# Kernel tuning notes

Measured on AMD Instinct MI355X. Metric: run time of the kernel, lower is better.

The kernel has to match this reference:

```python
import jax, jax.numpy as jnp
import numpy as np

L, N, C = 128, 32, 128
DIM_MLP, OUT = 128, 128


def setup_inputs() -> dict:
    key = jax.random.key(0)
    ks = jax.random.split(key, 6)
    s_in2 = 1.0 / np.sqrt(2 * C)
    s_mid = 1.0 / np.sqrt(DIM_MLP)
    s_in = 1.0 / np.sqrt(C)
    return {
        "x": jax.random.normal(ks[0], (L, N, C), jnp.float32),
        "attn_w1": jax.random.normal(ks[1], (2 * C, DIM_MLP), jnp.float32) * s_in2,
        "attn_b1": jnp.zeros((DIM_MLP,), jnp.float32),
        "attn_w2": jax.random.normal(ks[2], (DIM_MLP, OUT), jnp.float32) * s_mid,
        "attn_b2": jnp.zeros((OUT,), jnp.float32),
        "value_w1": jax.random.normal(ks[3], (C, DIM_MLP), jnp.float32) * s_in,
        "value_b1": jnp.zeros((DIM_MLP,), jnp.float32),
        "value_w2": jax.random.normal(ks[4], (DIM_MLP, OUT), jnp.float32) * s_mid,
        "value_b2": jnp.zeros((OUT,), jnp.float32),
    }


def reference(x, attn_w1, attn_b1, attn_w2, attn_b2,
              value_w1, value_b1, value_w2, value_b2):
    l, n, c = x.shape
    # Outer concat: pair[i, j, b] = concat(x[i, b], x[j, b])  -> (l, l, N, 2C)
    xi = jnp.broadcast_to(x[:, None, :, :], (l, l, n, c))
    xj = jnp.broadcast_to(x[None, :, :, :], (l, l, n, c))
    pair = jnp.concatenate([xi, xj], axis=-1)
    # Pairwise attention MLP (ReLU hidden, linear output)
    h = jax.nn.relu(pair @ attn_w1 + attn_b1)          # (l, l, N, dim_mlp)
    attn = h @ attn_w2 + attn_b2                       # (l, l, N, out)
    # Value MLP
    hv = jax.nn.relu(x @ value_w1 + value_b1)          # (l, N, dim_mlp)
    value = hv @ value_w2 + value_b2                   # (l, N, out)
    # Elementwise weighted reduce over key axis j (NOT a matmul over channels)
    out = jnp.einsum('ijbc,jbc->ibc', attn, value)     # (l, N, out)
    return out
```

## Files before the change

kernel.cpp:

```cpp
#include <hip/hip_runtime.h>
#include <hip/hip_bf16.h>

#define L_DIM 128
#define N_DIM 32
#define C_DIM 128
#define K_DIM 128
#define OUT_DIM 128

#define QV_STRIDE 132

typedef __attribute__((ext_vector_type(8))) short short8;
typedef __attribute__((ext_vector_type(4))) float float4v;

static __device__ __forceinline__ short bf16_bits(float f) {
    __bf16 h = (__bf16)f;
    return __builtin_bit_cast(short, h);
}

__global__ __launch_bounds__(256) void k_pre(
    const float* __restrict__ x,
    const float* __restrict__ attn_w1, const float* __restrict__ attn_b1,
    const float* __restrict__ attn_w2,
    const float* __restrict__ value_w1, const float* __restrict__ value_b1,
    const float* __restrict__ value_w2, const float* __restrict__ value_b2,
    float* __restrict__ P, float* __restrict__ Q, float* __restrict__ V,
    short* __restrict__ W2s)
{
    int bid = blockIdx.x;
    if (bid >= 512) {
        int e = (bid - 512) * 256 + threadIdx.x;
        int idx  = e & 7;
        int colr = (e >> 3) & 15;
        int quad = (e >> 7) & 3;
        int mi   = (e >> 9) & 3;
        int ct   = e >> 11;
        int k = quad * 8 + 32 * mi + idx;
        int c = ct * 16 + colr;
        W2s[e] = bf16_bits(attn_w2[k * OUT_DIM + c]);
        return;
    }

    __shared__ float xs[8][C_DIM];
    __shared__ float hvs[8][K_DIM];
    int tid = threadIdx.x;
    int r0  = bid * 8;

    {
        int f = tid * 4;
        int row = f >> 7, c = f & 127;
        *(float4v*)(&xs[row][c]) = *(const float4v*)(x + (r0 + row) * C_DIM + c);
    }
    __syncthreads();

    int ks   = tid & 127;
    int half = tid >> 7;

    float pacc[4] = {0,0,0,0};
    float qacc[4] = {0,0,0,0};
    float hacc[4] = {0,0,0,0};
    #pragma unroll 4
    for (int c = 0; c < C_DIM; ++c) {
        float wa = attn_w1[c * K_DIM + ks];
        float wb = attn_w1[(C_DIM + c) * K_DIM + ks];
        float wv = value_w1[c * K_DIM + ks];
        #pragma unroll
        for (int r = 0; r < 4; ++r) {
            float xr = xs[half * 4 + r][c];
            pacc[r] = fmaf(xr, wa, pacc[r]);
            qacc[r] = fmaf(xr, wb, qacc[r]);
            hacc[r] = fmaf(xr, wv, hacc[r]);
        }
    }
    float b1 = attn_b1[ks], vb1 = value_b1[ks];
    #pragma unroll
    for (int r = 0; r < 4; ++r) {
        int rr = r0 + half * 4 + r;
        int i = rr >> 5, bb = rr & 31;
        P[(bb * L_DIM + i) * K_DIM + ks] = pacc[r];
        Q[(bb * L_DIM + i) * K_DIM + ks] = qacc[r] + b1;
        hvs[half * 4 + r][ks] = fmaxf(hacc[r] + vb1, 0.f);
    }
    __syncthreads();

    float vacc[4] = {0,0,0,0};
    #pragma unroll 4
    for (int k = 0; k < K_DIM; ++k) {
        float w = value_w2[k * OUT_DIM + ks];
        #pragma unroll
        for (int r = 0; r < 4; ++r)
            vacc[r] = fmaf(hvs[half * 4 + r][k], w, vacc[r]);
    }
    float vb2 = value_b2[ks];
    #pragma unroll
    for (int r = 0; r < 4; ++r) {
        int rr = r0 + half * 4 + r;
        int i = rr >> 5, bb = rr & 31;
        V[(bb * L_DIM + i) * OUT_DIM + ks] = vacc[r] + vb2;
    }
}

__global__ __launch_bounds__(256)
__attribute__((amdgpu_waves_per_eu(3)))
void k_main(
    const float* __restrict__ P, const float* __restrict__ Q,
    const float* __restrict__ V,
    const short* __restrict__ W2s, const float* __restrict__ attn_b2,
    float* __restrict__ out)
{
    __shared__ float Q_lds[2][16 * QV_STRIDE];
    __shared__ float V_lds[2][16 * QV_STRIDE];
    __shared__ float P_lds[2 * K_DIM];

    int b     = blockIdx.x >> 6;
    int ipair = blockIdx.x & 63;
    int tid   = threadIdx.x;
    int wave  = tid >> 6;
    int lane  = tid & 63;
    int quad  = lane >> 4;
    int col   = lane & 15;
    int iw    = wave >> 1;
    int cth   = wave & 1;

    short8 bfrag[4][4];
    const short8* w2p = (const short8*)W2s;
    #pragma unroll
    for (int cl = 0; cl < 4; ++cl)
        #pragma unroll
        for (int mi = 0; mi < 4; ++mi)
            bfrag[cl][mi] =
                w2p[(((cth * 4 + cl) * 4 + mi) * 4 + quad) * 16 + col];

    if (tid < 64)
        *(float4v*)&P_lds[tid * 4] =
            *(const float4v*)(P + (b * L_DIM + ipair * 2 + (tid >> 5)) * K_DIM
                              + (tid & 31) * 4);

    int srow = tid >> 4;
    int sc8  = (tid & 15) * 8;
    const float* Qbase = Q + (size_t)(b * L_DIM) * K_DIM;
    const float* Vbase = V + (size_t)(b * L_DIM) * OUT_DIM;

    {
        const float* qp = Qbase + srow * K_DIM + sc8;
        const float* vp = Vbase + srow * OUT_DIM + sc8;
        float4v qa = *(const float4v*)qp, qb = *(const float4v*)(qp + 4);
        float4v va = *(const float4v*)vp, vb = *(const float4v*)(vp + 4);
        *(float4v*)&Q_lds[0][srow * QV_STRIDE + sc8]     = qa;
        *(float4v*)&Q_lds[0][srow * QV_STRIDE + sc8 + 4] = qb;
        *(float4v*)&V_lds[0][srow * QV_STRIDE + sc8]     = va;
        *(float4v*)&V_lds[0][srow * QV_STRIDE + sc8 + 4] = vb;
    }
    __syncthreads();

    float acc[4] = {0.f, 0.f, 0.f, 0.f};
    float sv[4]  = {0.f, 0.f, 0.f, 0.f};
    const float* Pw = &P_lds[iw * K_DIM];

    for (int r = 0; r < 8; ++r) {
        int cur = r & 1;

        float4v nqa, nqb, nva, nvb;
        if (r < 7) {
            const float* qp = Qbase + ((r + 1) * 16 + srow) * K_DIM + sc8;
            const float* vp = Vbase + ((r + 1) * 16 + srow) * OUT_DIM + sc8;
            nqa = *(const float4v*)qp; nqb = *(const float4v*)(qp + 4);
            nva = *(const float4v*)vp; nvb = *(const float4v*)(vp + 4);
        }

        short8 af[4];
        const float* Qc = &Q_lds[cur][col * QV_STRIDE + quad * 8];
        #pragma unroll
        for (int ksl = 0; ksl < 4; ++ksl) {
            float4v q0 = *(const float4v*)(Qc + ksl * 32);
            float4v q1 = *(const float4v*)(Qc + ksl * 32 + 4);
            float4v p0 = *(const float4v*)(Pw + ksl * 32 + quad * 8);
            float4v p1 = *(const float4v*)(Pw + ksl * 32 + quad * 8 + 4);
            float4v s0 = p0 + q0;
            float4v s1 = p1 + q1;
            short8 a;
            #pragma unroll
            for (int t = 0; t < 4; ++t) {
                a[t]     = bf16_bits(fmaxf(s0[t], 0.f));
                a[t + 4] = bf16_bits(fmaxf(s1[t], 0.f));
            }
            af[ksl] = a;
        }

        const float* Vc = &V_lds[cur][0];
        #pragma unroll
        for (int cl = 0; cl < 4; ++cl) {
            float4v c4 = {0.f, 0.f, 0.f, 0.f};
            #pragma unroll
            for (int ksl = 0; ksl < 4; ++ksl)
                c4 = __builtin_amdgcn_mfma_f32_16x16x32_bf16(
                        af[ksl], bfrag[cl][ksl], c4, 0, 0, 0);
            int cc = cth * 64 + cl * 16 + col;
            #pragma unroll
            for (int rr = 0; rr < 4; ++rr) {
                float v = Vc[(quad * 4 + rr) * QV_STRIDE + cc];
                acc[cl] = fmaf(c4[rr], v, acc[cl]);
                sv[cl] += v;
            }
        }

        if (r < 7) {
            int nxt = cur ^ 1;
            *(float4v*)&Q_lds[nxt][srow * QV_STRIDE + sc8]     = nqa;
            *(float4v*)&Q_lds[nxt][srow * QV_STRIDE + sc8 + 4] = nqb;
            *(float4v*)&V_lds[nxt][srow * QV_STRIDE + sc8]     = nva;
            *(float4v*)&V_lds[nxt][srow * QV_STRIDE + sc8 + 4] = nvb;
            __syncthreads();
        }
    }

    #pragma unroll
    for (int cl = 0; cl < 4; ++cl) {
        acc[cl] += __shfl_xor(acc[cl], 16, 64);
        acc[cl] += __shfl_xor(acc[cl], 32, 64);
        sv[cl]  += __shfl_xor(sv[cl], 16, 64);
        sv[cl]  += __shfl_xor(sv[cl], 32, 64);
    }

    if (quad == 0) {
        int ig = ipair * 2 + iw;
        #pragma unroll
        for (int cl = 0; cl < 4; ++cl) {
            int cc = cth * 64 + cl * 16 + col;
            out[(ig * N_DIM + b) * OUT_DIM + cc] = acc[cl] + attn_b2[cc] * sv[cl];
        }
    }
}

extern "C" void kernel_launch(void* const* d_in, const int* in_sizes, int n_in,
                              void* d_out, int out_size, void* d_ws, size_t ws_size,
                              hipStream_t stream)
{
    const float* x        = (const float*)d_in[0];
    const float* attn_w1  = (const float*)d_in[1];
    const float* attn_b1  = (const float*)d_in[2];
    const float* attn_w2  = (const float*)d_in[3];
    const float* attn_b2  = (const float*)d_in[4];
    const float* value_w1 = (const float*)d_in[5];
    const float* value_b1 = (const float*)d_in[6];
    const float* value_w2 = (const float*)d_in[7];
    const float* value_b2 = (const float*)d_in[8];
    float* out = (float*)d_out;

    float* ws  = (float*)d_ws;
    float* P   = ws;
    float* Q   = ws + 524288;
    float* V   = ws + 1048576;
    short* W2s = (short*)(ws + 1572864);

    k_pre<<<576, 256, 0, stream>>>(x, attn_w1, attn_b1, attn_w2,
                                   value_w1, value_b1, value_w2, value_b2,
                                   P, Q, V, W2s);
    k_main<<<2048, 256, 0, stream>>>(P, Q, V, W2s, attn_b2, out);
}
```

Baseline: 127.4 us.

## Process two query rows per wave, transpose V layout, hold P in registers

Each wave now handles two output rows i, so every staged Q/V tile and every W2 fragment load is reused across two MFMA chains, and the grid halves to 1024 blocks. V is written transposed by the pre-kernel so each lane reads its four V values with one vector LDS load instead of four scalar loads. P moves from LDS into registers, and the pre-kernel's x indexing is regrouped per batch. This costs more registers (launch bounds changed to 2 blocks per CU) and fewer blocks to hide latency.

```diff
diff --git a/kernel.cpp b/kernel.cpp
--- a/kernel.cpp
+++ b/kernel.cpp
@@ -7,7 +7,8 @@
 #define K_DIM 128
 #define OUT_DIM 128
 
-#define QV_STRIDE 132
+#define Q_STRIDE  132
+#define VT_STRIDE 20
 
 typedef __attribute__((ext_vector_type(8))) short short8;
 typedef __attribute__((ext_vector_type(4))) float float4v;
@@ -23,7 +24,7 @@
     const float* __restrict__ attn_w2,
     const float* __restrict__ value_w1, const float* __restrict__ value_b1,
     const float* __restrict__ value_w2, const float* __restrict__ value_b2,
-    float* __restrict__ P, float* __restrict__ Q, float* __restrict__ V,
+    float* __restrict__ P, float* __restrict__ Q, float* __restrict__ Vt,
     short* __restrict__ W2s)
 {
     int bid = blockIdx.x;
@@ -43,12 +44,14 @@
     __shared__ float xs[8][C_DIM];
     __shared__ float hvs[8][K_DIM];
     int tid = threadIdx.x;
-    int r0  = bid * 8;
+    int b   = bid >> 4;
+    int i0g = (bid & 15) * 8;
 
     {
         int f = tid * 4;
         int row = f >> 7, c = f & 127;
-        *(float4v*)(&xs[row][c]) = *(const float4v*)(x + (r0 + row) * C_DIM + c);
+        *(float4v*)(&xs[row][c]) =
+            *(const float4v*)(x + ((size_t)(i0g + row) * N_DIM + b) * C_DIM + c);
     }
     __syncthreads();
 
@@ -74,10 +77,9 @@
     float b1 = attn_b1[ks], vb1 = value_b1[ks];
     #pragma unroll
     for (int r = 0; r < 4; ++r) {
-        int rr = r0 + half * 4 + r;
-        int i = rr >> 5, bb = rr & 31;
-        P[(bb * L_DIM + i) * K_DIM + ks] = pacc[r];
-        Q[(bb * L_DIM + i) * K_DIM + ks] = qacc[r] + b1;
+        int i = i0g + half * 4 + r;
+        P[((size_t)b * L_DIM + i) * K_DIM + ks] = pacc[r];
+        Q[((size_t)b * L_DIM + i) * K_DIM + ks] = qacc[r] + b1;
         hvs[half * 4 + r][ks] = fmaxf(hacc[r] + vb1, 0.f);
     }
     __syncthreads();
@@ -91,35 +93,30 @@
             vacc[r] = fmaf(hvs[half * 4 + r][k], w, vacc[r]);
     }
     float vb2 = value_b2[ks];
-    #pragma unroll
-    for (int r = 0; r < 4; ++r) {
-        int rr = r0 + half * 4 + r;
-        int i = rr >> 5, bb = rr & 31;
-        V[(bb * L_DIM + i) * OUT_DIM + ks] = vacc[r] + vb2;
-    }
-}
-
-__global__ __launch_bounds__(256)
-__attribute__((amdgpu_waves_per_eu(3)))
+    float4v vout = { vacc[0] + vb2, vacc[1] + vb2, vacc[2] + vb2, vacc[3] + vb2 };
+    *(float4v*)(Vt + ((size_t)b * OUT_DIM + ks) * L_DIM + i0g + half * 4) = vout;
+}
+
+__global__ __launch_bounds__(256, 2)
 void k_main(
     const float* __restrict__ P, const float* __restrict__ Q,
-    const float* __restrict__ V,
+    const float* __restrict__ Vt,
     const short* __restrict__ W2s, const float* __restrict__ attn_b2,
     float* __restrict__ out)
 {
-    __shared__ float Q_lds[2][16 * QV_STRIDE];
-    __shared__ float V_lds[2][16 * QV_STRIDE];
-    __shared__ float P_lds[2 * K_DIM];
-
-    int b     = blockIdx.x >> 6;
-    int ipair = blockIdx.x & 63;
-    int tid   = threadIdx.x;
-    int wave  = tid >> 6;
-    int lane  = tid & 63;
-    int quad  = lane >> 4;
-    int col   = lane & 15;
-    int iw    = wave >> 1;
-    int cth   = wave & 1;
+    __shared__ float Q_lds[2][16 * Q_STRIDE];
+    __shared__ float Vt_lds[2][128 * VT_STRIDE];
+
+    int b    = blockIdx.x >> 5;
+    int it4  = blockIdx.x & 31;
+    int tid  = threadIdx.x;
+    int wave = tid >> 6;
+    int lane = tid & 63;
+    int quad = lane >> 4;
+    int col  = lane & 15;
+    int ip   = wave >> 1;
+    int cth  = wave & 1;
+    int i0   = it4 * 4 + ip * 2;
 
     short8 bfrag[4][4];
     const short8* w2p = (const short8*)W2s;
@@ -130,31 +127,39 @@
             bfrag[cl][mi] =
                 w2p[(((cth * 4 + cl) * 4 + mi) * 4 + quad) * 16 + col];
 
-    if (tid < 64)
-        *(float4v*)&P_lds[tid * 4] =
-            *(const float4v*)(P + (b * L_DIM + ipair * 2 + (tid >> 5)) * K_DIM
-                              + (tid & 31) * 4);
+    float4v pf[2][4][2];
+    #pragma unroll
+    for (int ii = 0; ii < 2; ++ii) {
+        const float* Pp = P + ((size_t)b * L_DIM + i0 + ii) * K_DIM + quad * 8;
+        #pragma unroll
+        for (int ksl = 0; ksl < 4; ++ksl) {
+            pf[ii][ksl][0] = *(const float4v*)(Pp + ksl * 32);
+            pf[ii][ksl][1] = *(const float4v*)(Pp + ksl * 32 + 4);
+        }
+    }
 
     int srow = tid >> 4;
     int sc8  = (tid & 15) * 8;
-    const float* Qbase = Q + (size_t)(b * L_DIM) * K_DIM;
-    const float* Vbase = V + (size_t)(b * L_DIM) * OUT_DIM;
+    int cs   = tid >> 1;
+    int ch   = (tid & 1) * 8;
+    const float* Qbase = Q  + (size_t)b * L_DIM * K_DIM;
+    const float* Vbase = Vt + (size_t)b * OUT_DIM * L_DIM;
 
     {
         const float* qp = Qbase + srow * K_DIM + sc8;
-        const float* vp = Vbase + srow * OUT_DIM + sc8;
         float4v qa = *(const float4v*)qp, qb = *(const float4v*)(qp + 4);
+        *(float4v*)&Q_lds[0][srow * Q_STRIDE + sc8]     = qa;
+        *(float4v*)&Q_lds[0][srow * Q_STRIDE + sc8 + 4] = qb;
+        const float* vp = Vbase + cs * L_DIM + ch;
         float4v va = *(const float4v*)vp, vb = *(const float4v*)(vp + 4);
-        *(float4v*)&Q_lds[0][srow * QV_STRIDE + sc8]     = qa;
-        *(float4v*)&Q_lds[0][srow * QV_STRIDE + sc8 + 4] = qb;
-        *(float4v*)&V_lds[0][srow * QV_STRIDE + sc8]     = va;
-        *(float4v*)&V_lds[0][srow * QV_STRIDE + sc8 + 4] = vb;
+        *(float4v*)&Vt_lds[0][cs * VT_STRIDE + ch]     = va;
+        *(float4v*)&Vt_lds[0][cs * VT_STRIDE + ch + 4] = vb;
     }
     __syncthreads();
 
-    float acc[4] = {0.f, 0.f, 0.f, 0.f};
-    float sv[4]  = {0.f, 0.f, 0.f, 0.f};
-    const float* Pw = &P_lds[iw * K_DIM];
+    float acc0[4] = {0.f, 0.f, 0.f, 0.f};
+    float acc1[4] = {0.f, 0.f, 0.f, 0.f};
+    float sv[4]   = {0.f, 0.f, 0.f, 0.f};
 
     for (int r = 0; r < 8; ++r) {
         int cur = r & 1;
@@ -162,71 +167,80 @@
         float4v nqa, nqb, nva, nvb;
         if (r < 7) {
             const float* qp = Qbase + ((r + 1) * 16 + srow) * K_DIM + sc8;
-            const float* vp = Vbase + ((r + 1) * 16 + srow) * OUT_DIM + sc8;
             nqa = *(const float4v*)qp; nqb = *(const float4v*)(qp + 4);
+            const float* vp = Vbase + cs * L_DIM + (r + 1) * 16 + ch;
             nva = *(const float4v*)vp; nvb = *(const float4v*)(vp + 4);
         }
 
-        short8 af[4];
-        const float* Qc = &Q_lds[cur][col * QV_STRIDE + quad * 8];
+        short8 af[2][4];
+        const float* Qc = &Q_lds[cur][col * Q_STRIDE + quad * 8];
         #pragma unroll
         for (int ksl = 0; ksl < 4; ++ksl) {
             float4v q0 = *(const float4v*)(Qc + ksl * 32);
             float4v q1 = *(const float4v*)(Qc + ksl * 32 + 4);
-            float4v p0 = *(const float4v*)(Pw + ksl * 32 + quad * 8);
-            float4v p1 = *(const float4v*)(Pw + ksl * 32 + quad * 8 + 4);
-            float4v s0 = p0 + q0;
-            float4v s1 = p1 + q1;
-            short8 a;
             #pragma unroll
-            for (int t = 0; t < 4; ++t) {
-                a[t]     = bf16_bits(fmaxf(s0[t], 0.f));
-                a[t + 4] = bf16_bits(fmaxf(s1[t], 0.f));
+            for (int ii = 0; ii < 2; ++ii) {
+                float4v s0 = pf[ii][ksl][0] + q0;
+                float4v s1 = pf[ii][ksl][1] + q1;
+                short8 a;
+                #pragma unroll
+                for (int t = 0; t < 4; ++t) {
+                    a[t]     = bf16_bits(fmaxf(s0[t], 0.f));
+                    a[t + 4] = bf16_bits(fmaxf(s1[t], 0.f));
+                }
+                af[ii][ksl] = a;
             }
-            af[ksl] = a;
-        }
-
-        const float* Vc = &V_lds[cur][0];
+        }
+
+        const float* Vc = &Vt_lds[cur][0];
         #pragma unroll
         for (int cl = 0; cl < 4; ++cl) {
-            float4v c4 = {0.f, 0.f, 0.f, 0.f};
+            float4v c40 = {0.f, 0.f, 0.f, 0.f};
+            float4v c41 = {0.f, 0.f, 0.f, 0.f};
             #pragma unroll
-            for (int ksl = 0; ksl < 4; ++ksl)
-                c4 = __builtin_amdgcn_mfma_f32_16x16x32_bf16(
-                        af[ksl], bfrag[cl][ksl], c4, 0, 0, 0);
+            for (int ksl = 0; ksl < 4; ++ksl) {
+                c40 = __builtin_amdgcn_mfma_f32_16x16x32_bf16(
+                        af[0][ksl], bfrag[cl][ksl], c40, 0, 0, 0);
+                c41 = __builtin_amdgcn_mfma_f32_16x16x32_bf16(
+                        af[1][ksl], bfrag[cl][ksl], c41, 0, 0, 0);
+            }
             int cc = cth * 64 + cl * 16 + col;
+            float4v vv = *(const float4v*)(Vc + cc * VT_STRIDE + quad * 4);
             #pragma unroll
             for (int rr = 0; rr < 4; ++rr) {
-                float v = Vc[(quad * 4 + rr) * QV_STRIDE + cc];
-                acc[cl] = fmaf(c4[rr], v, acc[cl]);
-                sv[cl] += v;
+                acc0[cl] = fmaf(c40[rr], vv[rr], acc0[cl]);
+                acc1[cl] = fmaf(c41[rr], vv[rr], acc1[cl]);
+                sv[cl]  += vv[rr];
             }
         }
 
         if (r < 7) {
             int nxt = cur ^ 1;
-            *(float4v*)&Q_lds[nxt][srow * QV_STRIDE + sc8]     = nqa;
-            *(float4v*)&Q_lds[nxt][srow * QV_STRIDE + sc8 + 4] = nqb;
-            *(float4v*)&V_lds[nxt][srow * QV_STRIDE + sc8]     = nva;
-            *(float4v*)&V_lds[nxt][srow * QV_STRIDE + sc8 + 4] = nvb;
+            *(float4v*)&Q_lds[nxt][srow * Q_STRIDE + sc8]      = nqa;
+            *(float4v*)&Q_lds[nxt][srow * Q_STRIDE + sc8 + 4]  = nqb;
+            *(float4v*)&Vt_lds[nxt][cs * VT_STRIDE + ch]       = nva;
+            *(float4v*)&Vt_lds[nxt][cs * VT_STRIDE + ch + 4]   = nvb;
             __syncthreads();
         }
     }
 
     #pragma unroll
     for (int cl = 0; cl < 4; ++cl) {
-        acc[cl] += __shfl_xor(acc[cl], 16, 64);
-        acc[cl] += __shfl_xor(acc[cl], 32, 64);
-        sv[cl]  += __shfl_xor(sv[cl], 16, 64);
-        sv[cl]  += __shfl_xor(sv[cl], 32, 64);
+        acc0[cl] += __shfl_xor(acc0[cl], 16, 64);
+        acc0[cl] += __shfl_xor(acc0[cl], 32, 64);
+        acc1[cl] += __shfl_xor(acc1[cl], 16, 64);
+        acc1[cl] += __shfl_xor(acc1[cl], 32, 64);
+        sv[cl]   += __shfl_xor(sv[cl], 16, 64);
+        sv[cl]   += __shfl_xor(sv[cl], 32, 64);
     }
 
     if (quad == 0) {
-        int ig = ipair * 2 + iw;
         #pragma unroll
         for (int cl = 0; cl < 4; ++cl) {
             int cc = cth * 64 + cl * 16 + col;
-            out[(ig * N_DIM + b) * OUT_DIM + cc] = acc[cl] + attn_b2[cc] * sv[cl];
+            float bsv = attn_b2[cc] * sv[cl];
+            out[((size_t)i0 * N_DIM + b) * OUT_DIM + cc]       = acc0[cl] + bsv;
+            out[((size_t)(i0 + 1) * N_DIM + b) * OUT_DIM + cc] = acc1[cl] + bsv;
         }
     }
 }
@@ -249,11 +263,11 @@
     float* ws  = (float*)d_ws;
     float* P   = ws;
     float* Q   = ws + 524288;
-    float* V   = ws + 1048576;
+    float* Vt  = ws + 1048576;
     short* W2s = (short*)(ws + 1572864);
 
     k_pre<<<576, 256, 0, stream>>>(x, attn_w1, attn_b1, attn_w2,
                                    value_w1, value_b1, value_w2, value_b2,
-                                   P, Q, V, W2s);
-    k_main<<<2048, 256, 0, stream>>>(P, Q, V, W2s, attn_b2, out);
-}
+                                   P, Q, Vt, W2s);
+    k_main<<<1024, 256, 0, stream>>>(P, Q, Vt, W2s, attn_b2, out);
+}
```

New measurement: 126.1 us. About the same (-1.0%).
